# Optimization experiments

Hardware: AMD Instinct MI355X
Metric: run time of the kernel (lower is better)

## Reference

```python
import jax, jax.numpy as jnp
import numpy as np

N_USER, N_ITEM, D = 50000, 30000, 64
N = N_USER + N_ITEM
NNZ_UI, NNZ_R, NNZ_II = 1000000, 800000, 300000
IMG_F, TXT_F = 512, 384
EPS = 1e-5


def spmm(rows, cols, vals, x, n_out):
    # sparse [n_out, n_in] @ dense [n_in, d] via gather + segment-sum
    return jax.ops.segment_sum(vals[:, None] * x[cols], rows, num_segments=n_out)


def leaky_relu(x):
    return jnp.where(x >= 0, x, 0.01 * x)


def setup_inputs() -> dict:
    key = jax.random.key(0)
    ks = jax.random.split(key, 32)
    f = lambda i, shape, s=0.05: (jax.random.normal(ks[i], shape, dtype=jnp.float32) * s)
    inp = {
        'user_emb': f(0, (N_USER, D)),
        'item_emb': f(1, (N_ITEM, D)),
        'image_embedding': f(2, (N_ITEM, IMG_F), 1.0),
        'text_embedding': f(3, (N_ITEM, TXT_F), 1.0),
        'W_img': f(4, (IMG_F, D)), 'b_img': jnp.zeros((D,), jnp.float32),
        'bn_g_img': jnp.ones((D,), jnp.float32), 'bn_b_img': jnp.zeros((D,), jnp.float32),
        'W_txt': f(5, (TXT_F, D)), 'b_txt': jnp.zeros((D,), jnp.float32),
        'bn_g_txt': jnp.ones((D,), jnp.float32), 'bn_b_txt': jnp.zeros((D,), jnp.float32),
        'W_gate_img': f(6, (D, D)), 'b_gate_img': jnp.zeros((D,), jnp.float32),
        'W_gate_txt': f(7, (D, D)), 'b_gate_txt': jnp.zeros((D,), jnp.float32),
        'W_common1': f(8, (D, D)), 'b_common1': jnp.zeros((D,), jnp.float32),
        'w_common2': f(9, (D,)),
        'ui_vals': jax.random.uniform(ks[10], (NNZ_UI,), dtype=jnp.float32),
        'R_vals': jax.random.uniform(ks[11], (NNZ_R,), dtype=jnp.float32),
        'ii_img_vals': jax.random.uniform(ks[12], (NNZ_II,), dtype=jnp.float32),
        'ii_txt_vals': jax.random.uniform(ks[13], (NNZ_II,), dtype=jnp.float32),
        'ui_rows': jax.random.randint(ks[14], (NNZ_UI,), 0, N, dtype=jnp.int32),
        'ui_cols': jax.random.randint(ks[15], (NNZ_UI,), 0, N, dtype=jnp.int32),
        'R_rows': jax.random.randint(ks[16], (NNZ_R,), 0, N_USER, dtype=jnp.int32),
        'R_cols': jax.random.randint(ks[17], (NNZ_R,), 0, N_ITEM, dtype=jnp.int32),
        'ii_img_rows': jax.random.randint(ks[18], (NNZ_II,), 0, N_ITEM, dtype=jnp.int32),
        'ii_img_cols': jax.random.randint(ks[19], (NNZ_II,), 0, N_ITEM, dtype=jnp.int32),
        'ii_txt_rows': jax.random.randint(ks[20], (NNZ_II,), 0, N_ITEM, dtype=jnp.int32),
        'ii_txt_cols': jax.random.randint(ks[21], (NNZ_II,), 0, N_ITEM, dtype=jnp.int32),
    }
    return inp


def reference(user_emb, item_emb, image_embedding, text_embedding,
              W_img, b_img, bn_g_img, bn_b_img,
              W_txt, b_txt, bn_g_txt, bn_b_txt,
              W_gate_img, b_gate_img, W_gate_txt, b_gate_txt,
              W_common1, b_common1, w_common2,
              ui_vals, R_vals, ii_img_vals, ii_txt_vals,
              ui_rows, ui_cols, R_rows, R_cols,
              ii_img_rows, ii_img_cols, ii_txt_rows, ii_txt_cols):
    # ---- user_item_GCN: adj = original + diffusion (fused edge list) ----
    cat = jnp.concatenate([item_emb, user_emb], axis=0)  # [N, D], item first per source
    embs = [cat]
    for _ in range(2):
        cat = spmm(ui_rows, ui_cols, ui_vals, cat, N)
        embs.append(cat)
    content_embedding = jnp.stack(embs, axis=1).mean(axis=1)  # [N, D]

    # ---- modal projections (BN inference, dropout=eval identity) ----
    def project(x, W, b, g, beta):
        h = x @ W + b
        h = h * (g / jnp.sqrt(1.0 + EPS)) + beta  # BatchNorm1d, running stats (0, 1)
        return leaky_relu(h)

    img_feat = project(image_embedding, W_img, b_img, bn_g_img, bn_b_img)  # [I, D]
    txt_feat = project(text_embedding, W_txt, b_txt, bn_g_txt, bn_b_txt)

    # ---- item_item_GCN ----
    def modal_branch(feat, Wg, bg, rows, cols, vals):
        it = item_emb * jax.nn.sigmoid(feat @ Wg + bg)  # gated item embedding
        for _ in range(2):
            it = spmm(rows, cols, vals, it, N_ITEM)
        us = spmm(R_rows, R_cols, R_vals, it, N_USER)  # R @ item -> user
        return jnp.concatenate([us, it], axis=0)  # [N, D], user first per source

    image_ui = modal_branch(img_feat, W_gate_img, b_gate_img, ii_img_rows, ii_img_cols, ii_img_vals)
    text_ui = modal_branch(txt_feat, W_gate_txt, b_gate_txt, ii_txt_rows, ii_txt_cols, ii_txt_vals)

    # ---- gate_attention_fusion (non-tiktok: 2 modalities) ----
    def att_score(e):
        return leaky_relu(e @ W_common1 + b_common1) @ w_common2  # [N]

    att = jnp.stack([att_score(image_ui), att_score(text_ui)], axis=-1)  # [N, 2]
    w = jax.nn.softmax(att, axis=-1)
    common = w[:, 0:1] * image_ui + w[:, 1:2] * text_ui
    special_img = image_ui - common
    special_txt = text_ui - common

    return jnp.stack([content_embedding, special_img, special_txt, common], axis=0)  # [4, N, D]
```

## Files before the change

### kernel.cpp

```cpp
#include <hip/hip_runtime.h>

#define N_USER 50000
#define N_ITEM 30000
#define DIM    64
#define NTOT   80000
#define NNZ_UI 1000000
#define NNZ_R  800000
#define NNZ_II 300000
#define IMG_F  512
#define TXT_F  384

#define NROWS_ALL 190000
#define NNZ_ALL   2400000
#define BASE_R    NTOT
#define BASE_II   (NTOT + N_USER)
#define BASE_IT   (NTOT + N_USER + N_ITEM)

#define RB_BITS   9
#define RB_ROWS   512
#define NBUCK     ((NROWS_ALL + RB_ROWS - 1) / RB_ROWS)
#define NBLK_A2   400
#define EDG_A2    6000

#define NBLK_PG   625
#define NBLK_I16  1875
#define NBLK_U16  3125

__device__ __forceinline__ int edge_row(int i,
        const int* __restrict__ r0, const int* __restrict__ r1,
        const int* __restrict__ r2, const int* __restrict__ r3){
    if (i < NNZ_UI)                       return r0[i];
    if (i < NNZ_UI + NNZ_R)               return BASE_R  + r1[i - NNZ_UI];
    if (i < NNZ_UI + NNZ_R + NNZ_II)      return BASE_II + r2[i - NNZ_UI - NNZ_R];
    return BASE_IT + r3[i - NNZ_UI - NNZ_R - NNZ_II];
}

__device__ __forceinline__ void edge_all(int i,
        const int* __restrict__ r0, const int* __restrict__ c0, const float* __restrict__ v0,
        const int* __restrict__ r1, const int* __restrict__ c1, const float* __restrict__ v1,
        const int* __restrict__ r2, const int* __restrict__ c2, const float* __restrict__ v2,
        const int* __restrict__ r3, const int* __restrict__ c3, const float* __restrict__ v3,
        int& gr, int& col, float& val){
    if (i < NNZ_UI){
        gr = r0[i]; col = c0[i]; val = v0[i];
    } else if (i < NNZ_UI + NNZ_R){
        int j = i - NNZ_UI;               gr = BASE_R  + r1[j]; col = c1[j]; val = v1[j];
    } else if (i < NNZ_UI + NNZ_R + NNZ_II){
        int j = i - NNZ_UI - NNZ_R;       gr = BASE_II + r2[j]; col = c2[j]; val = v2[j];
    } else {
        int j = i - NNZ_UI - NNZ_R - NNZ_II; gr = BASE_IT + r3[j]; col = c3[j]; val = v3[j];
    }
}

__global__ __launch_bounds__(256) void k_bhist(const int* __restrict__ r0,
        const int* __restrict__ r1, const int* __restrict__ r2,
        const int* __restrict__ r3, int* __restrict__ bcnt){
    __shared__ int h[NBUCK];
    for (int i = threadIdx.x; i < NBUCK; i += 256) h[i] = 0;
    __syncthreads();
    const int stride = gridDim.x * 256;
    for (int i = blockIdx.x * 256 + threadIdx.x; i < NNZ_ALL; i += stride){
        int gr = edge_row(i, r0, r1, r2, r3);
        atomicAdd(&h[gr >> RB_BITS], 1);
    }
    __syncthreads();
    for (int i = threadIdx.x; i < NBUCK; i += 256){
        int c = h[i];
        if (c) atomicAdd(&bcnt[i], c);
    }
}

__global__ __launch_bounds__(512) void k_bscan(const int* __restrict__ bcnt,
        int* __restrict__ bbase, int* __restrict__ off){
    __shared__ int sh[512];
    const int t = threadIdx.x;
    int v = (t < NBUCK) ? bcnt[t] : 0;
    sh[t] = v;
    __syncthreads();
    for (int d = 1; d < 512; d <<= 1){
        int u = (t >= d) ? sh[t - d] : 0;
        __syncthreads();
        sh[t] += u;
        __syncthreads();
    }
    if (t < NBUCK) bbase[t] = sh[t] - v;
    if (t == NBUCK - 1){
        bbase[NBUCK] = sh[t];
        off[NROWS_ALL] = sh[t];
    }
}

__global__ __launch_bounds__(256) void k_bin(
        const int* __restrict__ r0, const int* __restrict__ c0, const float* __restrict__ v0,
        const int* __restrict__ r1, const int* __restrict__ c1, const float* __restrict__ v1,
        const int* __restrict__ r2, const int* __restrict__ c2, const float* __restrict__ v2,
        const int* __restrict__ r3, const int* __restrict__ c3, const float* __restrict__ v3,
        const int* __restrict__ bbase, int* __restrict__ bcur,
        int2* __restrict__ binned){
    __shared__ int lofs[NBUCK];
    __shared__ int lcur[NBUCK];
    const int t = threadIdx.x;
    for (int i = t; i < NBUCK; i += 256){ lofs[i] = 0; lcur[i] = 0; }
    __syncthreads();
    const int s0 = blockIdx.x * EDG_A2, s1 = s0 + EDG_A2;
    for (int i = s0 + t; i < s1; i += 256){
        int gr = edge_row(i, r0, r1, r2, r3);
        atomicAdd(&lofs[gr >> RB_BITS], 1);
    }
    __syncthreads();
    for (int i = t; i < NBUCK; i += 256){
        int c = lofs[i];
        lofs[i] = c ? (bbase[i] + atomicAdd(&bcur[i], c)) : 0;
    }
    __syncthreads();
    for (int i = s0 + t; i < s1; i += 256){
        int gr, col; float val;
        edge_all(i, r0, c0, v0, r1, c1, v1, r2, c2, v2, r3, c3, v3, gr, col, val);
        int b = gr >> RB_BITS;
        int slot = atomicAdd(&lcur[b], 1);
        binned[lofs[b] + slot] = make_int2((col << RB_BITS) | (gr & (RB_ROWS - 1)),
                                           __float_as_int(val));
    }
}

__global__ __launch_bounds__(256) void k_scatter(const int* __restrict__ bbase,
        const int2* __restrict__ binned, int* __restrict__ off,
        int2* __restrict__ csr){
    __shared__ int h[RB_ROWS];
    const int t = threadIdx.x;
    const int b = blockIdx.x;
    const int base = bbase[b];
    const int nb = bbase[b + 1] - base;
    h[t] = 0; h[t + 256] = 0;
    __syncthreads();
    for (int i = t; i < nb; i += 256)
        atomicAdd(&h[binned[base + i].x & (RB_ROWS - 1)], 1);
    __syncthreads();
    if (t < 64){
        int v[8], s = 0;
#pragma unroll
        for (int k = 0; k < 8; ++k){ v[k] = h[t * 8 + k]; s += v[k]; }
        int incl = s;
#pragma unroll
        for (int d = 1; d < 64; d <<= 1){
            int u = __shfl_up(incl, d, 64);
            if (t >= d) incl += u;
        }
        int run = incl - s;
#pragma unroll
        for (int k = 0; k < 8; ++k){ int tmp = v[k]; h[t * 8 + k] = run; run += tmp; }
    }
    __syncthreads();
    const int row0 = b << RB_BITS;
    for (int i = t; i < RB_ROWS; i += 256){
        int r = row0 + i;
        if (r < NROWS_ALL) off[r] = base + h[i];
    }
    __syncthreads();
    for (int i = t; i < nb; i += 256){
        int2 rec = binned[base + i];
        int lr = rec.x & (RB_ROWS - 1);
        int slot = atomicAdd(&h[lr], 1);
        csr[base + slot] = make_int2(rec.x >> RB_BITS, rec.y);
    }
}

__global__ void k_cat0(const float* __restrict__ item, const float* __restrict__ user,
                       float* __restrict__ o1){
    int i = blockIdx.x * 256 + threadIdx.x;
    const int ITEMS = N_ITEM * DIM;
    o1[i] = (i < ITEMS) ? item[i] : user[i - ITEMS];
}

__device__ __forceinline__ void pull_body(const int* __restrict__ off,
        const int2* __restrict__ csr, const float* __restrict__ x,
        float* __restrict__ y, int r, int l){
    int s = off[r], e = off[r + 1];
    float4 a0 = {0.f, 0.f, 0.f, 0.f};
    float4 a1 = {0.f, 0.f, 0.f, 0.f};
    int j = s;
    for (; j + 2 <= e; j += 2){
        int2 e0 = csr[j];
        int2 e1 = csr[j + 1];
        float v0 = __int_as_float(e0.y);
        float v1 = __int_as_float(e1.y);
        const float4 x0 = *reinterpret_cast<const float4*>(x + ((long)e0.x << 6) + l);
        const float4 x1 = *reinterpret_cast<const float4*>(x + ((long)e1.x << 6) + l);
        a0.x = fmaf(v0, x0.x, a0.x);
        a0.y = fmaf(v0, x0.y, a0.y);
        a0.z = fmaf(v0, x0.z, a0.z);
        a0.w = fmaf(v0, x0.w, a0.w);
        a1.x = fmaf(v1, x1.x, a1.x);
        a1.y = fmaf(v1, x1.y, a1.y);
        a1.z = fmaf(v1, x1.z, a1.z);
        a1.w = fmaf(v1, x1.w, a1.w);
    }
    if (j < e){
        int2 e0 = csr[j];
        float v0 = __int_as_float(e0.y);
        const float4 x0 = *reinterpret_cast<const float4*>(x + ((long)e0.x << 6) + l);
        a0.x = fmaf(v0, x0.x, a0.x);
        a0.y = fmaf(v0, x0.y, a0.y);
        a0.z = fmaf(v0, x0.z, a0.z);
        a0.w = fmaf(v0, x0.w, a0.w);
    }
    a0.x += a1.x; a0.y += a1.y; a0.z += a1.z; a0.w += a1.w;
    *reinterpret_cast<float4*>(y + ((long)r << 6) + l) = a0;
}

__global__ void k_pull(const int* __restrict__ off, const int2* __restrict__ csr,
                       const float* __restrict__ x, float* __restrict__ y, int nrows){
    int t = blockIdx.x * 256 + threadIdx.x;
    int r = t >> 4;
    if (r >= nrows) return;
    pull_body(off, csr, x, y, r, (t & 15) << 2);
}

__global__ void k_pull2(const int* __restrict__ offA, const int2* __restrict__ csr,
                        const float* __restrict__ xA, float* __restrict__ yA,
                        const int* __restrict__ offB, const float* __restrict__ xB,
                        float* __restrict__ yB, int nrows, int nblk_half){
    int b = blockIdx.x;
    const int* off; const float* x; float* y;
    if (b < nblk_half){ off = offA; x = xA; y = yA; }
    else              { b -= nblk_half; off = offB; x = xB; y = yB; }
    int t = b * 256 + threadIdx.x;
    int r = t >> 4;
    if (r >= nrows) return;
    pull_body(off, csr, x, y, r, (t & 15) << 2);
}

__global__ void k_pull_mean(const int* __restrict__ off, const int2* __restrict__ csr,
                            const float* __restrict__ x, const float* __restrict__ a,
                            float* __restrict__ o0, int nrows){
    int t = blockIdx.x * 256 + threadIdx.x;
    int r = t >> 4;
    if (r >= nrows) return;
    int l = (t & 15) << 2;
    int s = off[r], e = off[r + 1];
    float4 a0 = {0.f, 0.f, 0.f, 0.f};
    float4 a1 = {0.f, 0.f, 0.f, 0.f};
    int j = s;
    for (; j + 2 <= e; j += 2){
        int2 e0 = csr[j];
        int2 e1 = csr[j + 1];
        float v0 = __int_as_float(e0.y);
        float v1 = __int_as_float(e1.y);
        const float4 x0 = *reinterpret_cast<const float4*>(x + ((long)e0.x << 6) + l);
        const float4 x1 = *reinterpret_cast<const float4*>(x + ((long)e1.x << 6) + l);
        a0.x = fmaf(v0, x0.x, a0.x);
        a0.y = fmaf(v0, x0.y, a0.y);
        a0.z = fmaf(v0, x0.z, a0.z);
        a0.w = fmaf(v0, x0.w, a0.w);
        a1.x = fmaf(v1, x1.x, a1.x);
        a1.y = fmaf(v1, x1.y, a1.y);
        a1.z = fmaf(v1, x1.z, a1.z);
        a1.w = fmaf(v1, x1.w, a1.w);
    }
    if (j < e){
        int2 e0 = csr[j];
        float v0 = __int_as_float(e0.y);
        const float4 x0 = *reinterpret_cast<const float4*>(x + ((long)e0.x << 6) + l);
        a0.x = fmaf(v0, x0.x, a0.x);
        a0.y = fmaf(v0, x0.y, a0.y);
        a0.z = fmaf(v0, x0.z, a0.z);
        a0.w = fmaf(v0, x0.w, a0.w);
    }
    const float4 av = *reinterpret_cast<const float4*>(a + ((long)r << 6) + l);
    const float4 xv = *reinterpret_cast<const float4*>(x + ((long)r << 6) + l);
    float4 o;
    o.x = (av.x + xv.x + a0.x + a1.x) * (1.0f / 3.0f);
    o.y = (av.y + xv.y + a0.y + a1.y) * (1.0f / 3.0f);
    o.z = (av.z + xv.z + a0.z + a1.z) * (1.0f / 3.0f);
    o.w = (av.w + xv.w + a0.w + a1.w) * (1.0f / 3.0f);
    *reinterpret_cast<float4*>(o0 + ((long)r << 6) + l) = o;
}

__global__ __launch_bounds__(256) void k_projgate3(
        const float* __restrict__ Xi, const float* __restrict__ Wi,
        const float* __restrict__ bi, const float* __restrict__ gi,
        const float* __restrict__ bei, const float* __restrict__ Wgi,
        const float* __restrict__ bgi,
        const float* __restrict__ Xt, const float* __restrict__ Wt,
        const float* __restrict__ bt, const float* __restrict__ gt,
        const float* __restrict__ bet, const float* __restrict__ Wgt,
        const float* __restrict__ bgt,
        const float* __restrict__ item,
        float* __restrict__ Pi, float* __restrict__ Pt){
    __shared__ float xs[48][68];
    __shared__ float ws[64][64];
    const int t  = threadIdx.x;
    const int tr = t >> 4;
    const int tc = t & 15;

    const bool isTxt = blockIdx.x >= NBLK_PG;
    const int  blk   = isTxt ? (blockIdx.x - NBLK_PG) : blockIdx.x;
    const int  K     = isTxt ? TXT_F : IMG_F;
    const float* X   = isTxt ? Xt  : Xi;
    const float* W   = isTxt ? Wt  : Wi;
    const float* bb  = isTxt ? bt  : bi;
    const float* gg  = isTxt ? gt  : gi;
    const float* be  = isTxt ? bet : bei;
    const float* Wg  = isTxt ? Wgt : Wgi;
    const float* bg  = isTxt ? bgt : bgi;
    float* outP      = isTxt ? Pt  : Pi;
    const int row0   = blk * 48;

    float acc[3][4];
#pragma unroll
    for (int i = 0; i < 3; ++i)
#pragma unroll
        for (int j = 0; j < 4; ++j) acc[i][j] = 0.f;

    for (int ks = 0; ks < K; ks += 64){
        __syncthreads();
#pragma unroll
        for (int i = 0; i < 3; ++i){
            int r = tr + 16 * i;
            *reinterpret_cast<float4*>(&xs[r][tc * 4]) =
                *reinterpret_cast<const float4*>(X + (long)(row0 + r) * K + ks + tc * 4);
        }
        {
            const float4* wsrc = reinterpret_cast<const float4*>(W + (long)ks * 64);
            float4* wdst = reinterpret_cast<float4*>(&ws[0][0]);
#pragma unroll
            for (int i = 0; i < 4; ++i) wdst[t + 256 * i] = wsrc[t + 256 * i];
        }
        __syncthreads();
#pragma unroll 8
        for (int kk = 0; kk < 64; kk += 2){
            float2 a[3];
#pragma unroll
            for (int i = 0; i < 3; ++i)
                a[i] = *reinterpret_cast<const float2*>(&xs[tr + 16 * i][kk]);
            float4 b0 = *reinterpret_cast<const float4*>(&ws[kk][tc * 4]);
            float4 b1 = *reinterpret_cast<const float4*>(&ws[kk + 1][tc * 4]);
#pragma unroll
            for (int i = 0; i < 3; ++i){
                acc[i][0] = fmaf(a[i].x, b0.x, acc[i][0]);
                acc[i][1] = fmaf(a[i].x, b0.y, acc[i][1]);
                acc[i][2] = fmaf(a[i].x, b0.z, acc[i][2]);
                acc[i][3] = fmaf(a[i].x, b0.w, acc[i][3]);
                acc[i][0] = fmaf(a[i].y, b1.x, acc[i][0]);
                acc[i][1] = fmaf(a[i].y, b1.y, acc[i][1]);
                acc[i][2] = fmaf(a[i].y, b1.z, acc[i][2]);
                acc[i][3] = fmaf(a[i].y, b1.w, acc[i][3]);
            }
        }
    }

    const float4 b4  = reinterpret_cast<const float4*>(bb)[tc];
    const float4 g4  = reinterpret_cast<const float4*>(gg)[tc];
    const float4 be4 = reinterpret_cast<const float4*>(be)[tc];
    __syncthreads();
#pragma unroll
    for (int i = 0; i < 3; ++i){
        int r = tr + 16 * i;
        float4 h;
        h.x = (acc[i][0] + b4.x) * (g4.x * 0.99999500003749943f) + be4.x;
        h.y = (acc[i][1] + b4.y) * (g4.y * 0.99999500003749943f) + be4.y;
        h.z = (acc[i][2] + b4.z) * (g4.z * 0.99999500003749943f) + be4.z;
        h.w = (acc[i][3] + b4.w) * (g4.w * 0.99999500003749943f) + be4.w;
        h.x = (h.x >= 0.f) ? h.x : 0.01f * h.x;
        h.y = (h.y >= 0.f) ? h.y : 0.01f * h.y;
        h.z = (h.z >= 0.f) ? h.z : 0.01f * h.z;
        h.w = (h.w >= 0.f) ? h.w : 0.01f * h.w;
        *reinterpret_cast<float4*>(&xs[r][tc * 4]) = h;
    }
    {
        const float4* wsrc = reinterpret_cast<const float4*>(Wg);
        float4* wdst = reinterpret_cast<float4*>(&ws[0][0]);
#pragma unroll
        for (int i = 0; i < 4; ++i) wdst[t + 256 * i] = wsrc[t + 256 * i];
    }
    __syncthreads();

    float ac2[3][4];
#pragma unroll
    for (int i = 0; i < 3; ++i)
#pragma unroll
        for (int j = 0; j < 4; ++j) ac2[i][j] = 0.f;
#pragma unroll 8
    for (int kk = 0; kk < 64; kk += 2){
        float2 a[3];
#pragma unroll
        for (int i = 0; i < 3; ++i)
            a[i] = *reinterpret_cast<const float2*>(&xs[tr + 16 * i][kk]);
        float4 b0 = *reinterpret_cast<const float4*>(&ws[kk][tc * 4]);
        float4 b1 = *reinterpret_cast<const float4*>(&ws[kk + 1][tc * 4]);
#pragma unroll
        for (int i = 0; i < 3; ++i){
            ac2[i][0] = fmaf(a[i].x, b0.x, ac2[i][0]);
            ac2[i][1] = fmaf(a[i].x, b0.y, ac2[i][1]);
            ac2[i][2] = fmaf(a[i].x, b0.z, ac2[i][2]);
            ac2[i][3] = fmaf(a[i].x, b0.w, ac2[i][3]);
            ac2[i][0] = fmaf(a[i].y, b1.x, ac2[i][0]);
            ac2[i][1] = fmaf(a[i].y, b1.y, ac2[i][1]);
            ac2[i][2] = fmaf(a[i].y, b1.z, ac2[i][2]);
            ac2[i][3] = fmaf(a[i].y, b1.w, ac2[i][3]);
        }
    }

    const float4 bg4 = reinterpret_cast<const float4*>(bg)[tc];
#pragma unroll
    for (int i = 0; i < 3; ++i){
        int r = tr + 16 * i;
        const float4 iv = *reinterpret_cast<const float4*>(
                item + (long)(row0 + r) * 64 + tc * 4);
        float4 o;
        o.x = iv.x / (1.f + __expf(-(ac2[i][0] + bg4.x)));
        o.y = iv.y / (1.f + __expf(-(ac2[i][1] + bg4.y)));
        o.z = iv.z / (1.f + __expf(-(ac2[i][2] + bg4.z)));
        o.w = iv.w / (1.f + __expf(-(ac2[i][3] + bg4.w)));
        *reinterpret_cast<float4*>(outP + (long)(row0 + r) * 64 + tc * 4) = o;
    }
}

__global__ __launch_bounds__(256) void k_fuse(const float* __restrict__ img,
        const float* __restrict__ txt, const float* __restrict__ W1,
        const float* __restrict__ b1, const float* __restrict__ w2,
        float* __restrict__ out){
    __shared__ float si[64][68];
    __shared__ float st[64][68];
    __shared__ float w1s[64][64];
    const int t  = threadIdx.x;
    const int tr = t >> 4;
    const int tc = t & 15;
    const long row0 = (long)blockIdx.x * 64;

#pragma unroll
    for (int i = 0; i < 4; ++i){
        int r = tr + 16 * i;
        *reinterpret_cast<float4*>(&si[r][tc * 4]) =
            *reinterpret_cast<const float4*>(img + (row0 + r) * 64 + tc * 4);
        *reinterpret_cast<float4*>(&st[r][tc * 4]) =
            *reinterpret_cast<const float4*>(txt + (row0 + r) * 64 + tc * 4);
    }
    {
        const float4* wsrc = reinterpret_cast<const float4*>(W1);
        float4* wdst = reinterpret_cast<float4*>(&w1s[0][0]);
#pragma unroll
        for (int i = 0; i < 4; ++i) wdst[t + 256 * i] = wsrc[t + 256 * i];
    }
    __syncthreads();

    float ai[4][4], at[4][4];
#pragma unroll
    for (int i = 0; i < 4; ++i)
#pragma unroll
        for (int j = 0; j < 4; ++j){ ai[i][j] = 0.f; at[i][j] = 0.f; }

#pragma unroll 8
    for (int kk = 0; kk < 64; kk += 2){
        float4 b0 = *reinterpret_cast<const float4*>(&w1s[kk][tc * 4]);
        float4 b1v = *reinterpret_cast<const float4*>(&w1s[kk + 1][tc * 4]);
#pragma unroll
        for (int i = 0; i < 4; ++i){
            float2 a = *reinterpret_cast<const float2*>(&si[tr + 16 * i][kk]);
            float2 c = *reinterpret_cast<const float2*>(&st[tr + 16 * i][kk]);
            ai[i][0] = fmaf(a.x, b0.x, ai[i][0]);
            ai[i][1] = fmaf(a.x, b0.y, ai[i][1]);
            ai[i][2] = fmaf(a.x, b0.z, ai[i][2]);
            ai[i][3] = fmaf(a.x, b0.w, ai[i][3]);
            ai[i][0] = fmaf(a.y, b1v.x, ai[i][0]);
            ai[i][1] = fmaf(a.y, b1v.y, ai[i][1]);
            ai[i][2] = fmaf(a.y, b1v.z, ai[i][2]);
            ai[i][3] = fmaf(a.y, b1v.w, ai[i][3]);
            at[i][0] = fmaf(c.x, b0.x, at[i][0]);
            at[i][1] = fmaf(c.x, b0.y, at[i][1]);
            at[i][2] = fmaf(c.x, b0.z, at[i][2]);
            at[i][3] = fmaf(c.x, b0.w, at[i][3]);
            at[i][0] = fmaf(c.y, b1v.x, at[i][0]);
            at[i][1] = fmaf(c.y, b1v.y, at[i][1]);
            at[i][2] = fmaf(c.y, b1v.z, at[i][2]);
            at[i][3] = fmaf(c.y, b1v.w, at[i][3]);
        }
    }

    const float4 b14 = reinterpret_cast<const float4*>(b1)[tc];
    const float4 w24 = reinterpret_cast<const float4*>(w2)[tc];
    float pi[4], pt[4];
#pragma unroll
    for (int i = 0; i < 4; ++i){
        float hi0 = ai[i][0] + b14.x; hi0 = (hi0 >= 0.f) ? hi0 : 0.01f * hi0;
        float hi1 = ai[i][1] + b14.y; hi1 = (hi1 >= 0.f) ? hi1 : 0.01f * hi1;
        float hi2 = ai[i][2] + b14.z; hi2 = (hi2 >= 0.f) ? hi2 : 0.01f * hi2;
        float hi3 = ai[i][3] + b14.w; hi3 = (hi3 >= 0.f) ? hi3 : 0.01f * hi3;
        float ht0 = at[i][0] + b14.x; ht0 = (ht0 >= 0.f) ? ht0 : 0.01f * ht0;
        float ht1 = at[i][1] + b14.y; ht1 = (ht1 >= 0.f) ? ht1 : 0.01f * ht1;
        float ht2 = at[i][2] + b14.z; ht2 = (ht2 >= 0.f) ? ht2 : 0.01f * ht2;
        float ht3 = at[i][3] + b14.w; ht3 = (ht3 >= 0.f) ? ht3 : 0.01f * ht3;
        pi[i] = fmaf(hi0, w24.x, fmaf(hi1, w24.y, fmaf(hi2, w24.z, hi3 * w24.w)));
        pt[i] = fmaf(ht0, w24.x, fmaf(ht1, w24.y, fmaf(ht2, w24.z, ht3 * w24.w)));
    }
#pragma unroll
    for (int m = 1; m < 16; m <<= 1){
#pragma unroll
        for (int i = 0; i < 4; ++i){
            pi[i] += __shfl_xor(pi[i], m, 64);
            pt[i] += __shfl_xor(pt[i], m, 64);
        }
    }

    const long NTD = (long)NTOT * DIM;
#pragma unroll
    for (int i = 0; i < 4; ++i){
        int r = tr + 16 * i;
        float mx = fmaxf(pi[i], pt[i]);
        float ei = __expf(pi[i] - mx), et = __expf(pt[i] - mx);
        float inv = 1.f / (ei + et);
        float wi = ei * inv, wt = et * inv;
        const float4 ie = *reinterpret_cast<const float4*>(&si[r][tc * 4]);
        const float4 te = *reinterpret_cast<const float4*>(&st[r][tc * 4]);
        float4 cm, oi, ot;
        cm.x = wi * ie.x + wt * te.x;
        cm.y = wi * ie.y + wt * te.y;
        cm.z = wi * ie.z + wt * te.z;
        cm.w = wi * ie.w + wt * te.w;
        oi.x = ie.x - cm.x; oi.y = ie.y - cm.y; oi.z = ie.z - cm.z; oi.w = ie.w - cm.w;
        ot.x = te.x - cm.x; ot.y = te.y - cm.y; ot.z = te.z - cm.z; ot.w = te.w - cm.w;
        long o = (row0 + r) * 64 + tc * 4;
        *reinterpret_cast<float4*>(out + NTD + o)     = oi;
        *reinterpret_cast<float4*>(out + 2 * NTD + o) = ot;
        *reinterpret_cast<float4*>(out + 3 * NTD + o) = cm;
    }
}

extern "C" void kernel_launch(void* const* d_in, const int* in_sizes, int n_in,
                              void* d_out, int out_size, void* d_ws, size_t ws_size,
                              hipStream_t stream){
    const float* user_emb  = (const float*)d_in[0];
    const float* item_emb  = (const float*)d_in[1];
    const float* image_emb = (const float*)d_in[2];
    const float* text_emb  = (const float*)d_in[3];
    const float* W_img = (const float*)d_in[4];
    const float* b_img = (const float*)d_in[5];
    const float* g_img = (const float*)d_in[6];
    const float* be_img= (const float*)d_in[7];
    const float* W_txt = (const float*)d_in[8];
    const float* b_txt = (const float*)d_in[9];
    const float* g_txt = (const float*)d_in[10];
    const float* be_txt= (const float*)d_in[11];
    const float* W_gi  = (const float*)d_in[12];
    const float* b_gi  = (const float*)d_in[13];
    const float* W_gt  = (const float*)d_in[14];
    const float* b_gt  = (const float*)d_in[15];
    const float* W_c1  = (const float*)d_in[16];
    const float* b_c1  = (const float*)d_in[17];
    const float* w_c2  = (const float*)d_in[18];
    const float* ui_vals = (const float*)d_in[19];
    const float* R_vals  = (const float*)d_in[20];
    const float* ii_iv   = (const float*)d_in[21];
    const float* ii_tv   = (const float*)d_in[22];
    const int* ui_rows = (const int*)d_in[23];
    const int* ui_cols = (const int*)d_in[24];
    const int* R_rows  = (const int*)d_in[25];
    const int* R_cols  = (const int*)d_in[26];
    const int* ii_ir   = (const int*)d_in[27];
    const int* ii_ic   = (const int*)d_in[28];
    const int* ii_tr   = (const int*)d_in[29];
    const int* ii_tc   = (const int*)d_in[30];

    const long ND = (long)NTOT * DIM;
    const long ID = (long)N_ITEM * DIM;
    const long UD = (long)N_USER * DIM;

    float* out = (float*)d_out;
    float* o0 = out;
    float* o1 = out + ND;
    float* o2 = out + 2 * ND;
    float* o3 = out + 3 * ND;

    float* P_img = o3;
    float* P_txt = o3 + ID;
    float* Q_img = o2;
    float* Q_txt = o1;

    int2* binned = (int2*)o0;

    int2* csr   = (int2*)d_ws;
    int*  off   = (int*)(csr + NNZ_ALL);
    int*  bcnt  = off + NROWS_ALL + 4;
    int*  bcur  = bcnt + NBUCK;
    int*  bbase = bcur + NBUCK;

    hipMemsetAsync(bcnt, 0, 2 * NBUCK * sizeof(int), stream);
    k_bhist<<<512, 256, 0, stream>>>(ui_rows, R_rows, ii_ir, ii_tr, bcnt);
    k_bscan<<<1, 512, 0, stream>>>(bcnt, bbase, off);
    k_bin<<<NBLK_A2, 256, 0, stream>>>(
        ui_rows, ui_cols, ui_vals,  R_rows, R_cols, R_vals,
        ii_ir, ii_ic, ii_iv,        ii_tr, ii_tc, ii_tv,
        bbase, bcur, binned);
    k_scatter<<<NBUCK, 256, 0, stream>>>(bbase, binned, off, csr);

    const int* offUI = off;
    const int* offR  = off + BASE_R;
    const int* offI2 = off + BASE_II;
    const int* offT2 = off + BASE_IT;

    k_cat0<<<ND / 256, 256, 0, stream>>>(item_emb, user_emb, o1);
    k_pull<<<NTOT / 16, 256, 0, stream>>>(offUI, csr, o1, o2, NTOT);
    k_pull_mean<<<NTOT / 16, 256, 0, stream>>>(offUI, csr, o2, o1, o0, NTOT);

    k_projgate3<<<2 * NBLK_PG, 256, 0, stream>>>(
        image_emb, W_img, b_img, g_img, be_img, W_gi, b_gi,
        text_emb,  W_txt, b_txt, g_txt, be_txt, W_gt, b_gt,
        item_emb, P_img, P_txt);
    k_pull2<<<2 * NBLK_I16, 256, 0, stream>>>(
        offI2, csr, P_img, Q_img, offT2, P_txt, Q_txt, N_ITEM, NBLK_I16);
    k_pull2<<<2 * NBLK_I16, 256, 0, stream>>>(
        offI2, csr, Q_img, o1 + UD, offT2, Q_txt, o2 + UD, N_ITEM, NBLK_I16);
    k_pull2<<<2 * NBLK_U16, 256, 0, stream>>>(
        offR, csr, o1 + UD, o1, offR, o2 + UD, o2, N_USER, NBLK_U16);

    k_fuse<<<NTOT / 64, 256, 0, stream>>>(o1, o2, W_c1, b_c1, w_c2, out);
}
```

Measured before the change: 571.8 us.

## Fuse concat into UI pulls, co-launch hop1 with projection, merge R pulls

The explicit concat kernel is removed. The UI spmm pulls now read item and user embeddings directly through a row-select helper. The first UI hop is merged into the same launch as the projection/gate GEMM, so the gather-bound and compute-bound blocks can overlap. The two R-matrix pulls for image and text now share a single pass over the CSR edges, which halves the index reads. In exchange, the mega kernel's GEMM blocks share an occupancy footprint (shared memory) with the lightweight pull blocks, and the row-select adds a branch on every gather.

```diff
diff --git a/kernel.cpp b/kernel.cpp
--- a/kernel.cpp
+++ b/kernel.cpp
@@ -23,6 +23,7 @@
 #define EDG_A2    6000
 
 #define NBLK_PG   625
+#define NBLK_UIP  5000
 #define NBLK_I16  1875
 #define NBLK_U16  3125
 
@@ -165,11 +166,9 @@
     }
 }
 
-__global__ void k_cat0(const float* __restrict__ item, const float* __restrict__ user,
-                       float* __restrict__ o1){
-    int i = blockIdx.x * 256 + threadIdx.x;
-    const int ITEMS = N_ITEM * DIM;
-    o1[i] = (i < ITEMS) ? item[i] : user[i - ITEMS];
+__device__ __forceinline__ const float* cat_row(int c,
+        const float* __restrict__ item, const float* __restrict__ user){
+    return (c < N_ITEM) ? (item + ((long)c << 6)) : (user + ((long)(c - N_ITEM) << 6));
 }
 
 __device__ __forceinline__ void pull_body(const int* __restrict__ off,
@@ -208,12 +207,40 @@
     *reinterpret_cast<float4*>(y + ((long)r << 6) + l) = a0;
 }
 
-__global__ void k_pull(const int* __restrict__ off, const int2* __restrict__ csr,
-                       const float* __restrict__ x, float* __restrict__ y, int nrows){
-    int t = blockIdx.x * 256 + threadIdx.x;
-    int r = t >> 4;
-    if (r >= nrows) return;
-    pull_body(off, csr, x, y, r, (t & 15) << 2);
+__device__ __forceinline__ void pull_cat_body(const int* __restrict__ off,
+        const int2* __restrict__ csr, const float* __restrict__ item,
+        const float* __restrict__ user, float* __restrict__ y, int r, int l){
+    int s = off[r], e = off[r + 1];
+    float4 a0 = {0.f, 0.f, 0.f, 0.f};
+    float4 a1 = {0.f, 0.f, 0.f, 0.f};
+    int j = s;
+    for (; j + 2 <= e; j += 2){
+        int2 e0 = csr[j];
+        int2 e1 = csr[j + 1];
+        float v0 = __int_as_float(e0.y);
+        float v1 = __int_as_float(e1.y);
+        const float4 x0 = *reinterpret_cast<const float4*>(cat_row(e0.x, item, user) + l);
+        const float4 x1 = *reinterpret_cast<const float4*>(cat_row(e1.x, item, user) + l);
+        a0.x = fmaf(v0, x0.x, a0.x);
+        a0.y = fmaf(v0, x0.y, a0.y);
+        a0.z = fmaf(v0, x0.z, a0.z);
+        a0.w = fmaf(v0, x0.w, a0.w);
+        a1.x = fmaf(v1, x1.x, a1.x);
+        a1.y = fmaf(v1, x1.y, a1.y);
+        a1.z = fmaf(v1, x1.z, a1.z);
+        a1.w = fmaf(v1, x1.w, a1.w);
+    }
+    if (j < e){
+        int2 e0 = csr[j];
+        float v0 = __int_as_float(e0.y);
+        const float4 x0 = *reinterpret_cast<const float4*>(cat_row(e0.x, item, user) + l);
+        a0.x = fmaf(v0, x0.x, a0.x);
+        a0.y = fmaf(v0, x0.y, a0.y);
+        a0.z = fmaf(v0, x0.z, a0.z);
+        a0.w = fmaf(v0, x0.w, a0.w);
+    }
+    a0.x += a1.x; a0.y += a1.y; a0.z += a1.z; a0.w += a1.w;
+    *reinterpret_cast<float4*>(y + ((long)r << 6) + l) = a0;
 }
 
 __global__ void k_pull2(const int* __restrict__ offA, const int2* __restrict__ csr,
@@ -230,9 +257,58 @@
     pull_body(off, csr, x, y, r, (t & 15) << 2);
 }
 
-__global__ void k_pull_mean(const int* __restrict__ off, const int2* __restrict__ csr,
-                            const float* __restrict__ x, const float* __restrict__ a,
-                            float* __restrict__ o0, int nrows){
+__global__ void k_pullR(const int* __restrict__ off, const int2* __restrict__ csr,
+                        const float* __restrict__ xA, float* __restrict__ yA,
+                        const float* __restrict__ xB, float* __restrict__ yB,
+                        int nrows){
+    int t = blockIdx.x * 256 + threadIdx.x;
+    int r = t >> 4;
+    if (r >= nrows) return;
+    int l = (t & 15) << 2;
+    int s = off[r], e = off[r + 1];
+    float4 pA0 = {0.f,0.f,0.f,0.f}, pA1 = {0.f,0.f,0.f,0.f};
+    float4 pB0 = {0.f,0.f,0.f,0.f}, pB1 = {0.f,0.f,0.f,0.f};
+    int j = s;
+    for (; j + 2 <= e; j += 2){
+        int2 e0 = csr[j];
+        int2 e1 = csr[j + 1];
+        float v0 = __int_as_float(e0.y);
+        float v1 = __int_as_float(e1.y);
+        long o0 = ((long)e0.x << 6) + l;
+        long o1 = ((long)e1.x << 6) + l;
+        const float4 xa0 = *reinterpret_cast<const float4*>(xA + o0);
+        const float4 xa1 = *reinterpret_cast<const float4*>(xA + o1);
+        const float4 xb0 = *reinterpret_cast<const float4*>(xB + o0);
+        const float4 xb1 = *reinterpret_cast<const float4*>(xB + o1);
+        pA0.x = fmaf(v0, xa0.x, pA0.x); pA0.y = fmaf(v0, xa0.y, pA0.y);
+        pA0.z = fmaf(v0, xa0.z, pA0.z); pA0.w = fmaf(v0, xa0.w, pA0.w);
+        pA1.x = fmaf(v1, xa1.x, pA1.x); pA1.y = fmaf(v1, xa1.y, pA1.y);
+        pA1.z = fmaf(v1, xa1.z, pA1.z); pA1.w = fmaf(v1, xa1.w, pA1.w);
+        pB0.x = fmaf(v0, xb0.x, pB0.x); pB0.y = fmaf(v0, xb0.y, pB0.y);
+        pB0.z = fmaf(v0, xb0.z, pB0.z); pB0.w = fmaf(v0, xb0.w, pB0.w);
+        pB1.x = fmaf(v1, xb1.x, pB1.x); pB1.y = fmaf(v1, xb1.y, pB1.y);
+        pB1.z = fmaf(v1, xb1.z, pB1.z); pB1.w = fmaf(v1, xb1.w, pB1.w);
+    }
+    if (j < e){
+        int2 e0 = csr[j];
+        float v0 = __int_as_float(e0.y);
+        long o0 = ((long)e0.x << 6) + l;
+        const float4 xa0 = *reinterpret_cast<const float4*>(xA + o0);
+        const float4 xb0 = *reinterpret_cast<const float4*>(xB + o0);
+        pA0.x = fmaf(v0, xa0.x, pA0.x); pA0.y = fmaf(v0, xa0.y, pA0.y);
+        pA0.z = fmaf(v0, xa0.z, pA0.z); pA0.w = fmaf(v0, xa0.w, pA0.w);
+        pB0.x = fmaf(v0, xb0.x, pB0.x); pB0.y = fmaf(v0, xb0.y, pB0.y);
+        pB0.z = fmaf(v0, xb0.z, pB0.z); pB0.w = fmaf(v0, xb0.w, pB0.w);
+    }
+    pA0.x += pA1.x; pA0.y += pA1.y; pA0.z += pA1.z; pA0.w += pA1.w;
+    pB0.x += pB1.x; pB0.y += pB1.y; pB0.z += pB1.z; pB0.w += pB1.w;
+    *reinterpret_cast<float4*>(yA + ((long)r << 6) + l) = pA0;
+    *reinterpret_cast<float4*>(yB + ((long)r << 6) + l) = pB0;
+}
+
+__global__ void k_pull_mean_cat(const int* __restrict__ off, const int2* __restrict__ csr,
+        const float* __restrict__ x, const float* __restrict__ item,
+        const float* __restrict__ user, float* __restrict__ o0, int nrows){
     int t = blockIdx.x * 256 + threadIdx.x;
     int r = t >> 4;
     if (r >= nrows) return;
@@ -266,7 +342,7 @@
         a0.z = fmaf(v0, x0.z, a0.z);
         a0.w = fmaf(v0, x0.w, a0.w);
     }
-    const float4 av = *reinterpret_cast<const float4*>(a + ((long)r << 6) + l);
+    const float4 av = *reinterpret_cast<const float4*>(cat_row(r, item, user) + l);
     const float4 xv = *reinterpret_cast<const float4*>(x + ((long)r << 6) + l);
     float4 o;
     o.x = (av.x + xv.x + a0.x + a1.x) * (1.0f / 3.0f);
@@ -276,7 +352,10 @@
     *reinterpret_cast<float4*>(o0 + ((long)r << 6) + l) = o;
 }
 
-__global__ __launch_bounds__(256) void k_projgate3(
+__global__ __launch_bounds__(256) void k_mega1(
+        const int* __restrict__ offUI, const int2* __restrict__ csr,
+        const float* __restrict__ user,
+        float* __restrict__ hop1out,
         const float* __restrict__ Xi, const float* __restrict__ Wi,
         const float* __restrict__ bi, const float* __restrict__ gi,
         const float* __restrict__ bei, const float* __restrict__ Wgi,
@@ -289,12 +368,20 @@
         float* __restrict__ Pi, float* __restrict__ Pt){
     __shared__ float xs[48][68];
     __shared__ float ws[64][64];
+
+    if (blockIdx.x < NBLK_UIP){
+        int t = blockIdx.x * 256 + threadIdx.x;
+        int r = t >> 4;
+        pull_cat_body(offUI, csr, item, user, hop1out, r, (t & 15) << 2);
+        return;
+    }
+
     const int t  = threadIdx.x;
     const int tr = t >> 4;
     const int tc = t & 15;
-
-    const bool isTxt = blockIdx.x >= NBLK_PG;
-    const int  blk   = isTxt ? (blockIdx.x - NBLK_PG) : blockIdx.x;
+    const int pgb = blockIdx.x - NBLK_UIP;
+    const bool isTxt = pgb >= NBLK_PG;
+    const int  blk   = isTxt ? (pgb - NBLK_PG) : pgb;
     const int  K     = isTxt ? TXT_F : IMG_F;
     const float* X   = isTxt ? Xt  : Xi;
     const float* W   = isTxt ? Wt  : Wi;
@@ -598,20 +685,21 @@
     const int* offI2 = off + BASE_II;
     const int* offT2 = off + BASE_IT;
 
-    k_cat0<<<ND / 256, 256, 0, stream>>>(item_emb, user_emb, o1);
-    k_pull<<<NTOT / 16, 256, 0, stream>>>(offUI, csr, o1, o2, NTOT);
-    k_pull_mean<<<NTOT / 16, 256, 0, stream>>>(offUI, csr, o2, o1, o0, NTOT);
-
-    k_projgate3<<<2 * NBLK_PG, 256, 0, stream>>>(
+    k_mega1<<<NBLK_UIP + 2 * NBLK_PG, 256, 0, stream>>>(
+        offUI, csr, user_emb, o2,
         image_emb, W_img, b_img, g_img, be_img, W_gi, b_gi,
         text_emb,  W_txt, b_txt, g_txt, be_txt, W_gt, b_gt,
         item_emb, P_img, P_txt);
+
+    k_pull_mean_cat<<<NBLK_UIP, 256, 0, stream>>>(
+        offUI, csr, o2, item_emb, user_emb, o0, NTOT);
+
     k_pull2<<<2 * NBLK_I16, 256, 0, stream>>>(
         offI2, csr, P_img, Q_img, offT2, P_txt, Q_txt, N_ITEM, NBLK_I16);
     k_pull2<<<2 * NBLK_I16, 256, 0, stream>>>(
         offI2, csr, Q_img, o1 + UD, offT2, Q_txt, o2 + UD, N_ITEM, NBLK_I16);
-    k_pull2<<<2 * NBLK_U16, 256, 0, stream>>>(
-        offR, csr, o1 + UD, o1, offR, o2 + UD, o2, N_USER, NBLK_U16);
+    k_pullR<<<NBLK_U16, 256, 0, stream>>>(
+        offR, csr, o1 + UD, o1, o2 + UD, o2, N_USER);
 
     k_fuse<<<NTOT / 64, 256, 0, stream>>>(o1, o2, W_c1, b_c1, w_c2, out);
 }
```

Result: no change. 562.9 us (-1.5%).
